# Kernel tuning notes

Hardware: AMD Instinct MI355X
Metric: run time of the kernel (lower is better)

Reference implementation:

```python
import jax, jax.numpy as jnp
import numpy as np

B, N = 16, 8192          # batch, number of points
IN_DIM, NDIM = 3, 2      # feature dim, spatial dim
K = 128                  # number of Fourier modes
C = 128                  # channel width (all layers equal)
L = 4                    # number of spectral layers
FC, OUT = 128, 1         # projection dims


def setup_inputs() -> dict:
    key = jax.random.key(0)
    ks = jax.random.split(key, 14)
    scale = 1.0 / (C * C)
    x = jax.random.uniform(ks[0], (B, N, IN_DIM + NDIM + 2), dtype=jnp.float32)
    modes = jax.random.normal(ks[1], (K, NDIM), dtype=jnp.float32) * (2.0 * jnp.pi)
    fc0_w = jax.random.normal(ks[2], (IN_DIM, C), dtype=jnp.float32) * 0.1
    fc0_b = jax.random.normal(ks[3], (C,), dtype=jnp.float32) * 0.1
    wc = scale * jax.random.uniform(ks[4], (L, C, C, K), dtype=jnp.float32)
    ws = scale * jax.random.uniform(ks[5], (L, C, C, K), dtype=jnp.float32)
    w0 = scale * jax.random.uniform(ks[6], (L, C, C, 1), dtype=jnp.float32)
    conv_w = jax.random.normal(ks[7], (L, C, C), dtype=jnp.float32) * 0.05  # Conv1d k=1 -> (out,in)
    conv_b = jax.random.normal(ks[8], (L, C), dtype=jnp.float32) * 0.05
    fc1_w = jax.random.normal(ks[9], (C, FC), dtype=jnp.float32) * 0.05
    fc1_b = jax.random.normal(ks[10], (FC,), dtype=jnp.float32) * 0.05
    fc2_w = jax.random.normal(ks[11], (FC, OUT), dtype=jnp.float32) * 0.05
    fc2_b = jax.random.normal(ks[12], (OUT,), dtype=jnp.float32) * 0.05
    return {"x": x, "modes": modes, "fc0_w": fc0_w, "fc0_b": fc0_b,
            "wc": wc, "ws": ws, "w0": w0, "conv_w": conv_w, "conv_b": conv_b,
            "fc1_w": fc1_w, "fc1_b": fc1_b, "fc2_w": fc2_w, "fc2_b": fc2_b}


def _gelu(v):
    return jax.nn.gelu(v, approximate=False)  # torch F.gelu default = exact erf


def reference(x, modes, fc0_w, fc0_b, wc, ws, w0, conv_w, conv_b, fc1_w, fc1_b, fc2_w, fc2_b):
    # aux channels: grid(ndim), weights(1), mask(1)
    aux = jnp.transpose(x[..., -(NDIM + 2):], (0, 2, 1))  # (b, ndim+2, N)
    grid = aux[:, :NDIM, :]
    weights = aux[:, NDIM:NDIM + 1, :]
    mask = aux[:, NDIM + 1:, :]
    size = grid.shape[-1]

    temp = jnp.einsum('bdx,kd->bkx', grid, modes)  # (b,k,N)
    bases_c = jnp.cos(temp) * mask
    bases_s = jnp.sin(temp) * mask
    bases_0 = mask                                  # (b,1,N)
    wsz = weights * size
    wbases_c, wbases_s, wbases_0 = bases_c * wsz, bases_s * wsz, bases_0 * wsz

    h = jnp.einsum('bxi,ic->bcx', x[..., :IN_DIM], fc0_w) + fc0_b[None, :, None]

    for l in range(L):
        # forward non-uniform transform
        x_c = jnp.einsum('bix,bkx->bik', h, wbases_c)
        x_s = -jnp.einsum('bix,bkx->bik', h, wbases_s)
        x_0 = jnp.einsum('bix,bkx->bik', h, wbases_0)
        Wc, Ws, W0 = wc[l] / size, ws[l] / size, w0[l] / size
        f_c = jnp.einsum('bik,iok->bok', x_c, Wc) - jnp.einsum('bik,iok->bok', x_s, Ws)
        f_s = jnp.einsum('bik,iok->bok', x_s, Wc) + jnp.einsum('bik,iok->bok', x_c, Ws)
        f_0 = jnp.einsum('bik,iok->bok', x_0, W0)
        # inverse transform
        x1 = (jnp.einsum('bok,bkx->box', f_0, bases_0)
              + 2.0 * jnp.einsum('bok,bkx->box', f_c, bases_c)
              - 2.0 * jnp.einsum('bok,bkx->box', f_s, bases_s))
        # pointwise 1x1 conv skip path
        x2 = jnp.einsum('oi,bix->box', conv_w[l], h) + conv_b[l][None, :, None]
        h = x1 + x2
        if l != L - 1:
            h = _gelu(h)

    y = jnp.transpose(h, (0, 2, 1))  # (b, N, C)
    y = _gelu(y @ fc1_w + fc1_b)
    y = y @ fc2_w + fc2_b
    return y
```

## Files before the change

kernel.cpp:

```cpp
#include <hip/hip_runtime.h>
#include <math.h>

#define BB 16
#define NN 8192
#define CC 128
#define KK 128
#define LL 4

#define APX 40
#define BPX 136

typedef short bf16x8 __attribute__((ext_vector_type(8)));
typedef float f32x4 __attribute__((ext_vector_type(4)));

typedef unsigned short u16;
typedef unsigned int u32;

__device__ __forceinline__ float gelu_f(float v){
  const float t = __builtin_amdgcn_exp2f(-2.45546696f * v);
  return v * __builtin_amdgcn_rcpf(1.0f + t);
}

__device__ __forceinline__ u16 f2bf(float f){
  u32 u = __float_as_uint(f);
  return (u16)((u + 0x7FFFu + ((u >> 16) & 1u)) >> 16);
}
__device__ __forceinline__ float bf2f(u16 u){ return __uint_as_float(((u32)u) << 16); }
__device__ __forceinline__ u32 pk2(float a, float b){
  return (u32)f2bf(a) | ((u32)f2bf(b) << 16);
}

__device__ __forceinline__ void gll16(const u16* g, u16* l){
  __builtin_amdgcn_global_load_lds(
      (const __attribute__((address_space(1))) void*)g,
      (__attribute__((address_space(3))) void*)l, 16, 0, 0);
}

__global__ __launch_bounds__(256) void bases_kernel(
    const float* __restrict__ X, const float* __restrict__ modes,
    u16* __restrict__ bcs, u16* __restrict__ bss,
    u16* __restrict__ bcT, u16* __restrict__ bsT,
    float* __restrict__ mA, float* __restrict__ sm2)
{
  __shared__ float smodes[2*KK];
  __shared__ u16 shc[64*BPX];
  __shared__ u16 shs[64*BPX];
  __shared__ float ssv[64];
  const int b = blockIdx.x;
  const int x0 = blockIdx.y*64;
  const int t = threadIdx.x;
  smodes[t] = modes[t];
  const int xl = t & 63;
  const int kq = t >> 6;
  const int x = x0 + xl;
  const float* xp = X + ((size_t)b*NN + x)*7;
  const float g0 = xp[3], g1 = xp[4], wv = xp[5], mv = xp[6];
  const float sv = wv * (float)NN;
  if (kq == 0){
    mA[b*NN + x] = mv;
    sm2[b*NN + x] = mv * sv;
    ssv[xl] = sv;
  }
  __syncthreads();
  #pragma unroll 4
  for (int kk = 0; kk < 32; ++kk){
    const int k = kq*32 + kk;
    const float tt = g0*smodes[2*k] + g1*smodes[2*k+1];
    float sn, cs;
    __sincosf(tt, &sn, &cs);
    shc[xl*BPX + k] = f2bf(cs*mv);
    shs[xl*BPX + k] = f2bf(sn*mv);
  }
  __syncthreads();
  for (int idx = t; idx < 64*16; idx += 256){
    const int row = idx >> 4, c16 = (idx & 15)*8;
    const size_t dst = ((size_t)b*NN + x0 + row)*KK + c16;
    *(uint4*)&bcT[dst] = *(const uint4*)&shc[row*BPX + c16];
    *(uint4*)&bsT[dst] = *(const uint4*)&shs[row*BPX + c16];
  }
  for (int idx = t; idx < 128*8; idx += 256){
    const int k = idx >> 3, x8 = (idx & 7)*8;
    uint4 vc, vs;
    u32* pc = (u32*)&vc;
    u32* ps = (u32*)&vs;
    #pragma unroll
    for (int e = 0; e < 4; ++e){
      const int xa = x8 + 2*e, xb2 = x8 + 2*e + 1;
      const float sa = ssv[xa], sb = ssv[xb2];
      pc[e] = pk2(bf2f(shc[xa*BPX+k])*sa, bf2f(shc[xb2*BPX+k])*sb);
      ps[e] = pk2(bf2f(shs[xa*BPX+k])*sa, bf2f(shs[xb2*BPX+k])*sb);
    }
    const size_t dst = ((size_t)b*KK + k)*NN + x0 + x8;
    *(uint4*)&bcs[dst] = vc;
    *(uint4*)&bss[dst] = vs;
  }
}

__global__ __launch_bounds__(256) void cvt_kernel(
    const float* __restrict__ convw, const float* __restrict__ fc1w,
    u16* __restrict__ cwb, u16* __restrict__ w1T)
{
  const int blk = blockIdx.x;
  const int t = threadIdx.x;
  if (blk < 64){
    const int base = blk*1024 + t*4;
    const float4 v = *(const float4*)&convw[base];
    ushort4 o;
    o.x = f2bf(v.x); o.y = f2bf(v.y); o.z = f2bf(v.z); o.w = f2bf(v.w);
    *(ushort4*)&cwb[base] = o;
  } else {
    const int i = (blk - 64)*1024 + t*4;
    const int f = i >> 7, c = i & 127;
    ushort4 o;
    o.x = f2bf(fc1w[(size_t)(c+0)*CC + f]);
    o.y = f2bf(fc1w[(size_t)(c+1)*CC + f]);
    o.z = f2bf(fc1w[(size_t)(c+2)*CC + f]);
    o.w = f2bf(fc1w[(size_t)(c+3)*CC + f]);
    *(ushort4*)&w1T[i] = o;
  }
}

__global__ __launch_bounds__(256) void fc0_kernel(
    const float* __restrict__ X, const float* __restrict__ w, const float* __restrict__ bias,
    const float* __restrict__ sm2,
    u16* __restrict__ hT, u16* __restrict__ hI, float* __restrict__ x0out)
{
  __shared__ float sxin[3*128];
  __shared__ float sw[3*128];
  __shared__ float sb[128];
  __shared__ float ssm2[128];
  __shared__ u16 sht[128*BPX];
  const int b = blockIdx.x;
  const int x0 = blockIdx.y*128;
  const int t = threadIdx.x;
  if (t < 128){
    sb[t] = bias[t];
    ssm2[t] = sm2[(size_t)b*NN + x0 + t];
    #pragma unroll
    for (int j = 0; j < 3; ++j){
      sw[j*128 + t] = w[j*128 + t];
      sxin[j*128 + t] = X[((size_t)b*NN + x0 + t)*7 + j];
    }
  }
  __syncthreads();
  const int o = t >> 1;
  const int xh = (t & 1)*64;
  const float w0v = sw[o], w1v = sw[128+o], w2v = sw[256+o], bv = sb[o];
  float xacc = 0.f;
  for (int x = xh; x < xh + 64; ++x){
    const float v = bv + sxin[x]*w0v + sxin[128+x]*w1v + sxin[256+x]*w2v;
    sht[o*BPX + x] = f2bf(v);
    xacc += v * ssm2[x];
  }
  xacc += __shfl_xor(xacc, 1);
  if ((t & 1) == 0) atomicAdd(&x0out[b*CC + o], xacc);
  __syncthreads();
  for (int idx = t; idx < 128*16; idx += 256){
    const int o2 = idx >> 4, x8 = (idx & 15)*8;
    *(uint4*)&hI[((size_t)b*CC + o2)*NN + x0 + x8] = *(const uint4*)&sht[o2*BPX + x8];
  }
  {
    const int x = t >> 1, oh = (t & 1)*64;
    #pragma unroll 2
    for (int j = 0; j < 8; ++j){
      const int ob = oh + j*8;
      uint4 qv;
      qv.x = (u32)sht[(ob+0)*BPX + x] | ((u32)sht[(ob+1)*BPX + x] << 16);
      qv.y = (u32)sht[(ob+2)*BPX + x] | ((u32)sht[(ob+3)*BPX + x] << 16);
      qv.z = (u32)sht[(ob+4)*BPX + x] | ((u32)sht[(ob+5)*BPX + x] << 16);
      qv.w = (u32)sht[(ob+6)*BPX + x] | ((u32)sht[(ob+7)*BPX + x] << 16);
      *(uint4*)&hT[((size_t)b*NN + x0 + x)*CC + ob] = qv;
    }
  }
}

template<int STORE>
__global__ __launch_bounds__(256) void proj_kernel(
    const u16* __restrict__ hI, const u16* __restrict__ bcs, const u16* __restrict__ bss,
    float* __restrict__ xc, float* __restrict__ xs)
{
  __shared__ u16 sa [2][128*32];
  __shared__ u16 sbc[2][128*32];
  __shared__ u16 sbs[2][128*32];
  const int b = blockIdx.x;
  const int z = blockIdx.y;
  const int t = threadIdx.x;
  const int w = t >> 6, l = t & 63, lm = l & 15, q = l >> 4;
  const int rr = l >> 2, c8 = (l & 3)*8;
  const u16* Asrc = hI + (size_t)b*CC*NN + z*512;
  const u16* Bc   = bcs + (size_t)b*KK*NN + z*512;
  const u16* Bs   = bss + (size_t)b*KK*NN + z*512;
  const f32x4 z4 = {0.f,0.f,0.f,0.f};
  f32x4 accC[2][8], accS[2][8];
  #pragma unroll
  for (int mt = 0; mt < 2; ++mt)
    #pragma unroll
    for (int nt = 0; nt < 8; ++nt){ accC[mt][nt] = z4; accS[mt][nt] = z4; }

  #pragma unroll
  for (int j = 0; j < 2; ++j){
    const int r = w*32 + j*16 + rr;
    gll16(Asrc + (size_t)r*NN + c8, sa [0] + (w*32 + j*16)*32);
    gll16(Bc   + (size_t)r*NN + c8, sbc[0] + (w*32 + j*16)*32);
    gll16(Bs   + (size_t)r*NN + c8, sbs[0] + (w*32 + j*16)*32);
  }
  for (int cs = 0; cs < 16; ++cs){
    __syncthreads();
    const int cur = cs & 1;
    if (cs < 15){
      const int nb = cur ^ 1;
      const int c2 = (cs + 1)*32;
      #pragma unroll
      for (int j = 0; j < 2; ++j){
        const int r = w*32 + j*16 + rr;
        gll16(Asrc + (size_t)r*NN + c2 + c8, sa [nb] + (w*32 + j*16)*32);
        gll16(Bc   + (size_t)r*NN + c2 + c8, sbc[nb] + (w*32 + j*16)*32);
        gll16(Bs   + (size_t)r*NN + c2 + c8, sbs[nb] + (w*32 + j*16)*32);
      }
    }
    const bf16x8 af0 = *(const bf16x8*)&sa[cur][(w*32      + lm)*32 + q*8];
    const bf16x8 af1 = *(const bf16x8*)&sa[cur][(w*32 + 16 + lm)*32 + q*8];
    #pragma unroll
    for (int nt = 0; nt < 8; ++nt){
      const bf16x8 bfc = *(const bf16x8*)&sbc[cur][(nt*16 + lm)*32 + q*8];
      const bf16x8 bfs = *(const bf16x8*)&sbs[cur][(nt*16 + lm)*32 + q*8];
      accC[0][nt] = __builtin_amdgcn_mfma_f32_16x16x32_bf16(af0, bfc, accC[0][nt], 0, 0, 0);
      accC[1][nt] = __builtin_amdgcn_mfma_f32_16x16x32_bf16(af1, bfc, accC[1][nt], 0, 0, 0);
      accS[0][nt] = __builtin_amdgcn_mfma_f32_16x16x32_bf16(af0, bfs, accS[0][nt], 0, 0, 0);
      accS[1][nt] = __builtin_amdgcn_mfma_f32_16x16x32_bf16(af1, bfs, accS[1][nt], 0, 0, 0);
    }
  }
  if (STORE){
    const size_t pbase = ((size_t)z*BB + b)*CC*KK;
    #pragma unroll
    for (int mt = 0; mt < 2; ++mt){
      #pragma unroll
      for (int nt = 0; nt < 8; ++nt){
        const int k = nt*16 + lm;
        #pragma unroll
        for (int r = 0; r < 4; ++r){
          const int i = w*32 + mt*16 + q*4 + r;
          xc[pbase + (size_t)i*KK + k] = accC[mt][nt][r];
          xs[pbase + (size_t)i*KK + k] = accS[mt][nt][r];
        }
      }
    }
  } else {
    #pragma unroll
    for (int mt = 0; mt < 2; ++mt){
      #pragma unroll
      for (int nt = 0; nt < 8; ++nt){
        const int k = nt*16 + lm;
        #pragma unroll
        for (int r = 0; r < 4; ++r){
          const int i = w*32 + mt*16 + q*4 + r;
          atomicAdd(&xc[((size_t)b*CC + i)*KK + k],  accC[mt][nt][r]);
          atomicAdd(&xs[((size_t)b*CC + i)*KK + k], -accS[mt][nt][r]);
        }
      }
    }
  }
}

__global__ __launch_bounds__(128) void reduce_f0_kernel(
    const float* __restrict__ xcP, const float* __restrict__ xsP,
    float* __restrict__ xc, float* __restrict__ xs,
    const float* __restrict__ x0a, const float* __restrict__ w0l,
    float* __restrict__ f0b)
{
  const int blk = blockIdx.x;
  if (blk < 2048){
    const int k = threadIdx.x;
    const size_t off = (size_t)blk*KK + k;
    const size_t zstr = (size_t)BB*CC*KK;
    float sc_ = 0.f, ss_ = 0.f;
    #pragma unroll
    for (int z = 0; z < 16; ++z){
      sc_ += xcP[(size_t)z*zstr + off];
      ss_ += xsP[(size_t)z*zstr + off];
    }
    xc[off] = sc_;
    xs[off] = -ss_;
  } else {
    const int b = blk - 2048, o = threadIdx.x;
    float acc = 0.f;
    for (int i = 0; i < CC; ++i) acc += x0a[b*CC+i] * w0l[(size_t)i*CC + o];
    f0b[b*CC+o] = acc * (1.0f/(float)NN);
  }
}

__global__ __launch_bounds__(128) void f0_kernel(
    const float* __restrict__ x0a, const float* __restrict__ w0l, float* __restrict__ f0b)
{
  const int b = blockIdx.x, o = threadIdx.x;
  float acc = 0.f;
  for (int i = 0; i < CC; ++i) acc += x0a[b*CC+i] * w0l[(size_t)i*CC + o];
  f0b[b*CC+o] = acc * (1.0f/(float)NN);
}

__global__ __launch_bounds__(256) void mix_kernel(
    const float* __restrict__ xc, const float* __restrict__ xs,
    const float* __restrict__ wcl, const float* __restrict__ wsl,
    u16* __restrict__ fcb, u16* __restrict__ fsb)
{
  const int o  = blockIdx.x;
  const int kh = blockIdx.y;
  const int t = threadIdx.x;
  const int k = kh*64 + (t & 63);
  const int bq = t >> 6;
  float aC[4] = {0.f,0.f,0.f,0.f}, aS[4] = {0.f,0.f,0.f,0.f};
  const float* wcp = wcl + (size_t)o*KK + k;
  const float* wsp = wsl + (size_t)o*KK + k;
  const float* xcp = xc + ((size_t)(bq*4)*CC)*KK + k;
  const float* xsp = xs + ((size_t)(bq*4)*CC)*KK + k;
  #pragma unroll 2
  for (int i = 0; i < CC; ++i){
    const float wcv = wcp[(size_t)i*CC*KK];
    const float wsv = wsp[(size_t)i*CC*KK];
    #pragma unroll
    for (int jb = 0; jb < 4; ++jb){
      const float xcv = xcp[((size_t)jb*CC + i)*KK];
      const float xsv = xsp[((size_t)jb*CC + i)*KK];
      aC[jb] += xcv*wcv - xsv*wsv;
      aS[jb] += xsv*wcv + xcv*wsv;
    }
  }
  const float sc = 2.0f/(float)NN;
  #pragma unroll
  for (int jb = 0; jb < 4; ++jb){
    const int b = bq*4 + jb;
    fcb[((size_t)b*CC + o)*KK + k] = f2bf( aC[jb]*sc);
    fsb[((size_t)b*CC + o)*KK + k] = f2bf(-aS[jb]*sc);
  }
}

__global__ __launch_bounds__(512) void fused_kernel(
    const u16* __restrict__ bcT, const u16* __restrict__ bsT, u16* __restrict__ hT,
    const u16* __restrict__ fcb, const u16* __restrict__ fsb,
    const u16* __restrict__ cwb, const float* __restrict__ cb,
    const float* __restrict__ f0b, const float* __restrict__ mA, const float* __restrict__ sm2,
    u16* __restrict__ hI, float* __restrict__ x0next, const int act)
{
  __shared__ u16 smem[24576];
  __shared__ float sm[256], ssm2[256], sf0[128], scb[128];
  const int b  = blockIdx.x;
  const int x0 = blockIdx.y*256;
  const int t = threadIdx.x;
  const int w = t >> 6, l = t & 63, lm = l & 15, q = l >> 4;
  const int lr = l >> 2, lc8 = (l & 3)*8;
  if (t < 256){
    sm[t]   = mA[(size_t)b*NN + x0 + t];
    ssm2[t] = sm2[(size_t)b*NN + x0 + t];
  }
  if (t < 128){
    sf0[t]  = f0b[b*CC + t];
    scb[t]  = cb[t];
  }
  const u16* Asrc0 = bcT + ((size_t)b*NN + x0)*KK;
  const u16* Asrc1 = bsT + ((size_t)b*NN + x0)*KK;
  const u16* Asrc2 = hT  + ((size_t)b*NN + x0)*CC;
  const u16* Bsrc0 = fcb + (size_t)b*CC*KK;
  const u16* Bsrc1 = fsb + (size_t)b*CC*KK;
  const f32x4 z4 = {0.f,0.f,0.f,0.f};
  f32x4 acc[2][8];
  #pragma unroll
  for (int mt = 0; mt < 2; ++mt)
    #pragma unroll
    for (int nt = 0; nt < 8; ++nt) acc[mt][nt] = z4;

  {
    const int ar = w*16 + lr;
    gll16(Asrc0 + (size_t)ar*128 + lc8,         smem + w*512);
    gll16(Asrc0 + (size_t)(ar+128)*128 + lc8,   smem + 4096 + w*512);
    gll16(Bsrc0 + (size_t)ar*128 + lc8,         smem + 16384 + w*512);
  }
  for (int s = 0; s < 12; ++s){
    __syncthreads();
    const int curA = (s & 1)*8192;
    const int curB = 16384 + (s & 1)*4096;
    if (s < 11){
      const int s1 = s + 1;
      const int g = s1 >> 2, kk = (s1 & 3)*32;
      const u16* Ap = (g == 0) ? Asrc0 : (g == 1) ? Asrc1 : Asrc2;
      const u16* Bp = (g == 0) ? Bsrc0 : (g == 1) ? Bsrc1 : cwb;
      const int nbA = (s1 & 1)*8192;
      const int nbB = 16384 + (s1 & 1)*4096;
      const int ar = w*16 + lr;
      gll16(Ap + (size_t)ar*128 + kk + lc8,       smem + nbA + w*512);
      gll16(Ap + (size_t)(ar+128)*128 + kk + lc8, smem + nbA + 4096 + w*512);
      gll16(Bp + (size_t)ar*128 + kk + lc8,       smem + nbB + w*512);
    }
    const bf16x8 af0 = *(const bf16x8*)&smem[curA + (w*32      + lm)*32 + q*8];
    const bf16x8 af1 = *(const bf16x8*)&smem[curA + (w*32 + 16 + lm)*32 + q*8];
    #pragma unroll
    for (int nt = 0; nt < 8; ++nt){
      const bf16x8 bf = *(const bf16x8*)&smem[curB + (nt*16 + lm)*32 + q*8];
      acc[0][nt] = __builtin_amdgcn_mfma_f32_16x16x32_bf16(af0, bf, acc[0][nt], 0, 0, 0);
      acc[1][nt] = __builtin_amdgcn_mfma_f32_16x16x32_bf16(af1, bf, acc[1][nt], 0, 0, 0);
    }
  }
  #pragma unroll
  for (int pass = 0; pass < 2; ++pass){
    __syncthreads();
    if ((w >> 2) == pass){
      float xpart[8];
      #pragma unroll
      for (int nt = 0; nt < 8; ++nt) xpart[nt] = 0.f;
      const int wl = w & 3;
      #pragma unroll
      for (int mt = 0; mt < 2; ++mt){
        const int xg = w*32 + mt*16 + q*4;
        const int xl = wl*32 + mt*16 + q*4;
        #pragma unroll
        for (int nt = 0; nt < 8; ++nt){
          const int o = nt*16 + lm;
          const float f0v = sf0[o], cbv = scb[o];
          float v0 = acc[mt][nt][0] + f0v*sm[xg+0] + cbv;
          float v1 = acc[mt][nt][1] + f0v*sm[xg+1] + cbv;
          float v2 = acc[mt][nt][2] + f0v*sm[xg+2] + cbv;
          float v3 = acc[mt][nt][3] + f0v*sm[xg+3] + cbv;
          if (act){ v0 = gelu_f(v0); v1 = gelu_f(v1); v2 = gelu_f(v2); v3 = gelu_f(v3); }
          smem[(xl+0)*BPX + o] = f2bf(v0);
          smem[(xl+1)*BPX + o] = f2bf(v1);
          smem[(xl+2)*BPX + o] = f2bf(v2);
          smem[(xl+3)*BPX + o] = f2bf(v3);
          if (act){
            uint2 st;
            st.x = pk2(v0, v1);
            st.y = pk2(v2, v3);
            *(uint2*)&hI[((size_t)b*CC + o)*NN + x0 + xg] = st;
            xpart[nt] += v0*ssm2[xg+0] + v1*ssm2[xg+1] + v2*ssm2[xg+2] + v3*ssm2[xg+3];
          }
        }
      }
      if (act){
        #pragma unroll
        for (int nt = 0; nt < 8; ++nt){
          float v = xpart[nt];
          v += __shfl_xor(v, 16);
          v += __shfl_xor(v, 32);
          if (q == 0) atomicAdd(&x0next[b*CC + nt*16 + lm], v);
        }
      }
    }
    __syncthreads();
    {
      const int xr = t >> 2;
      const int oq = (t & 3)*32;
      const size_t dst = ((size_t)b*NN + x0 + pass*128 + xr)*CC + oq;
      #pragma unroll
      for (int j = 0; j < 4; ++j){
        const uint4 v = *(const uint4*)&smem[xr*BPX + oq + j*8];
        *(uint4*)&hT[dst + j*8] = v;
      }
    }
  }
}

__global__ __launch_bounds__(256) void final_kernel(
    const u16* __restrict__ hT, const u16* __restrict__ w1T,
    const float* __restrict__ b1, const float* __restrict__ w2, const float* __restrict__ b2,
    float* __restrict__ out)
{
  __shared__ u16 sa[128*APX];
  __shared__ u16 sbt[128*APX];
  __shared__ float sb1[128], sw2[128];
  const int b  = blockIdx.x;
  const int x0 = blockIdx.y*128;
  const int t = threadIdx.x;
  const int w = t >> 6, l = t & 63, lm = l & 15, q = l >> 4;
  if (t < 128){ sb1[t] = b1[t]; sw2[t] = w2[t]; }
  const float b2v = b2[0];
  const f32x4 z4 = {0.f,0.f,0.f,0.f};
  f32x4 acc[2][8];
  #pragma unroll
  for (int mt = 0; mt < 2; ++mt)
    #pragma unroll
    for (int nt = 0; nt < 8; ++nt) acc[mt][nt] = z4;
  const u16* Ap = hT + ((size_t)b*NN + x0)*CC;
  const int row = t >> 2, ch = (t & 3)*8;
  for (int s = 0; s < 4; ++s){
    const int kk = s*32;
    __syncthreads();
    #pragma unroll
    for (int h = 0; h < 2; ++h){
      const int r = row + h*64;
      *(uint4*)&sa [r*APX + ch] = *(const uint4*)&Ap [(size_t)r*CC + kk + ch];
      *(uint4*)&sbt[r*APX + ch] = *(const uint4*)&w1T[(size_t)r*CC + kk + ch];
    }
    __syncthreads();
    bf16x8 af[2];
    af[0] = *(const bf16x8*)&sa[(w*32      + lm)*APX + q*8];
    af[1] = *(const bf16x8*)&sa[(w*32 + 16 + lm)*APX + q*8];
    #pragma unroll
    for (int nt = 0; nt < 8; ++nt){
      const bf16x8 bf = *(const bf16x8*)&sbt[(nt*16 + lm)*APX + q*8];
      acc[0][nt] = __builtin_amdgcn_mfma_f32_16x16x32_bf16(af[0], bf, acc[0][nt], 0, 0, 0);
      acc[1][nt] = __builtin_amdgcn_mfma_f32_16x16x32_bf16(af[1], bf, acc[1][nt], 0, 0, 0);
    }
  }
  #pragma unroll
  for (int mt = 0; mt < 2; ++mt){
    #pragma unroll
    for (int r = 0; r < 4; ++r){
      float s = 0.f;
      #pragma unroll
      for (int nt = 0; nt < 8; ++nt){
        const int f = nt*16 + lm;
        s += gelu_f(acc[mt][nt][r] + sb1[f]) * sw2[f];
      }
      s += __shfl_xor(s, 1);
      s += __shfl_xor(s, 2);
      s += __shfl_xor(s, 4);
      s += __shfl_xor(s, 8);
      if (lm == 0){
        const int x = x0 + w*32 + mt*16 + q*4 + r;
        out[(size_t)b*NN + x] = s + b2v;
      }
    }
  }
}

extern "C" void kernel_launch(void* const* d_in, const int* in_sizes, int n_in,
                              void* d_out, int out_size, void* d_ws, size_t ws_size,
                              hipStream_t stream)
{
  const float* X     = (const float*)d_in[0];
  const float* modes = (const float*)d_in[1];
  const float* fc0w  = (const float*)d_in[2];
  const float* fc0b  = (const float*)d_in[3];
  const float* wc    = (const float*)d_in[4];
  const float* wsm   = (const float*)d_in[5];
  const float* w0    = (const float*)d_in[6];
  const float* convw = (const float*)d_in[7];
  const float* convb = (const float*)d_in[8];
  const float* fc1w  = (const float*)d_in[9];
  const float* fc1b  = (const float*)d_in[10];
  const float* fc2w  = (const float*)d_in[11];
  const float* fc2b  = (const float*)d_in[12];
  float* out = (float*)d_out;

  const size_t nBKN = (size_t)BB*KK*NN;
  const size_t nBCK = (size_t)BB*CC*KK;
  const size_t nBC  = (size_t)BB*CC;
  const size_t nBN  = (size_t)BB*NN;

  const size_t need_A = 6*nBKN*2 + 2*(size_t)16*nBCK*4 + 2*nBCK*4 + 4*nBC*4
                      + 2*nBCK*2 + nBC*4 + 2*nBN*4 + (size_t)LL*CC*CC*2 + (size_t)CC*CC*2;
  const bool pathA = (ws_size >= need_A);

  char* p = (char*)d_ws;
  u16* bcs = (u16*)p; p += nBKN*2;
  u16* bss = (u16*)p; p += nBKN*2;
  u16* bcT = (u16*)p; p += nBKN*2;
  u16* bsT = (u16*)p; p += nBKN*2;
  u16* hI  = (u16*)p; p += nBKN*2;
  u16* hT  = (u16*)p; p += nBKN*2;
  float* xcP = nullptr; float* xsP = nullptr;
  if (pathA){
    xcP = (float*)p; p += (size_t)16*nBCK*4;
    xsP = (float*)p; p += (size_t)16*nBCK*4;
  }
  float* xcA = (float*)p; p += nBCK*4;
  float* xsA = (float*)p; p += nBCK*4;
  float* x0A = (float*)p; p += 4*nBC*4;
  u16* fcb = (u16*)p; p += nBCK*2;
  u16* fsb = (u16*)p; p += nBCK*2;
  float* f0b = (float*)p; p += nBC*4;
  float* mA  = (float*)p; p += nBN*4;
  float* sm2 = (float*)p; p += nBN*4;
  u16* cwb = (u16*)p; p += (size_t)LL*CC*CC*2;
  u16* w1T = (u16*)p; p += (size_t)CC*CC*2;

  hipMemsetAsync(x0A, 0, 4*nBC*sizeof(float), stream);
  cvt_kernel<<<dim3(80), 256, 0, stream>>>(convw, fc1w, cwb, w1T);
  bases_kernel<<<dim3(BB, NN/64), 256, 0, stream>>>(X, modes, bcs, bss, bcT, bsT, mA, sm2);
  fc0_kernel<<<dim3(BB, NN/128), 256, 0, stream>>>(X, fc0w, fc0b, sm2, hT, hI, x0A);

  for (int l = 0; l < LL; ++l){
    if (pathA){
      proj_kernel<1><<<dim3(BB, 16), 256, 0, stream>>>(hI, bcs, bss, xcP, xsP);
      reduce_f0_kernel<<<dim3(2048 + BB), 128, 0, stream>>>(xcP, xsP, xcA, xsA,
          x0A + (size_t)l*nBC, w0 + (size_t)l*CC*CC, f0b);
    } else {
      hipMemsetAsync(xcA, 0, 2*nBCK*sizeof(float), stream);
      proj_kernel<0><<<dim3(BB, 16), 256, 0, stream>>>(hI, bcs, bss, xcA, xsA);
      f0_kernel<<<dim3(BB), 128, 0, stream>>>(x0A + (size_t)l*nBC, w0 + (size_t)l*CC*CC, f0b);
    }
    mix_kernel<<<dim3(128, 2), 256, 0, stream>>>(xcA, xsA,
        wc + (size_t)l*CC*CC*KK, wsm + (size_t)l*CC*CC*KK, fcb, fsb);
    fused_kernel<<<dim3(BB, NN/256), 512, 0, stream>>>(
        bcT, bsT, hT, fcb, fsb,
        cwb + (size_t)l*CC*CC, convb + (size_t)l*CC,
        f0b, mA, sm2, hI,
        x0A + (size_t)(l+1 < LL ? l+1 : 0)*nBC,
        (l < LL-1) ? 1 : 0);
  }
  final_kernel<<<dim3(BB, NN/128), 256, 0, stream>>>(hT, w1T, fc1b, fc2w, fc2b, out);
}
```

Before: 711.7 us.

## Split projection kernel into cos/sin blocks with 512 threads each

The partial-sum projection path now launches a 512-thread kernel over a third grid dimension that selects the cosine or sine basis. Each block loads only the h tile and one basis tile and computes a single accumulator set per wave. This doubles the block count and cuts registers per thread, which should raise occupancy and parallelism. The cost is that the h tile is loaded twice, once per kind, which adds global traffic. The atomic path keeps the old kernel under a new name.

```diff
diff --git a/kernel.cpp b/kernel.cpp
--- a/kernel.cpp
+++ b/kernel.cpp
@@ -174,8 +174,57 @@
   }
 }
 
-template<int STORE>
-__global__ __launch_bounds__(256) void proj_kernel(
+__global__ __launch_bounds__(512) void proj512_kernel(
+    const u16* __restrict__ hI, const u16* __restrict__ bcs, const u16* __restrict__ bss,
+    float* __restrict__ xcP, float* __restrict__ xsP)
+{
+  __shared__ u16 sa[2][128*32];
+  __shared__ u16 sb[2][128*32];
+  const int b = blockIdx.x;
+  const int z = blockIdx.y;
+  const int kind = blockIdx.z;
+  const int t = threadIdx.x;
+  const int w = t >> 6, l = t & 63, lm = l & 15, q = l >> 4;
+  const int ar = t >> 2, ac8 = (t & 3)*8;
+  const u16* Asrc = hI + (size_t)b*CC*NN + z*512;
+  const u16* Bsrc = (kind ? bss : bcs) + (size_t)b*KK*NN + z*512;
+  const f32x4 z4 = {0.f,0.f,0.f,0.f};
+  f32x4 acc[8];
+  #pragma unroll
+  for (int nt = 0; nt < 8; ++nt) acc[nt] = z4;
+
+  gll16(Asrc + (size_t)ar*NN + ac8, sa[0] + w*512);
+  gll16(Bsrc + (size_t)ar*NN + ac8, sb[0] + w*512);
+  for (int cs = 0; cs < 16; ++cs){
+    __syncthreads();
+    const int cur = cs & 1;
+    if (cs < 15){
+      const int nb = cur ^ 1;
+      const int c2 = (cs + 1)*32;
+      gll16(Asrc + (size_t)ar*NN + c2 + ac8, sa[nb] + w*512);
+      gll16(Bsrc + (size_t)ar*NN + c2 + ac8, sb[nb] + w*512);
+    }
+    const bf16x8 af = *(const bf16x8*)&sa[cur][(w*16 + lm)*32 + q*8];
+    #pragma unroll
+    for (int nt = 0; nt < 8; ++nt){
+      const bf16x8 bf = *(const bf16x8*)&sb[cur][(nt*16 + lm)*32 + q*8];
+      acc[nt] = __builtin_amdgcn_mfma_f32_16x16x32_bf16(af, bf, acc[nt], 0, 0, 0);
+    }
+  }
+  float* outp = kind ? xsP : xcP;
+  const size_t pbase = ((size_t)z*BB + b)*CC*KK;
+  #pragma unroll
+  for (int nt = 0; nt < 8; ++nt){
+    const int k = nt*16 + lm;
+    #pragma unroll
+    for (int r = 0; r < 4; ++r){
+      const int i = w*16 + q*4 + r;
+      outp[pbase + (size_t)i*KK + k] = acc[nt][r];
+    }
+  }
+}
+
+__global__ __launch_bounds__(256) void proj_atomic_kernel(
     const u16* __restrict__ hI, const u16* __restrict__ bcs, const u16* __restrict__ bss,
     float* __restrict__ xc, float* __restrict__ xs)
 {
@@ -196,7 +245,6 @@
   for (int mt = 0; mt < 2; ++mt)
     #pragma unroll
     for (int nt = 0; nt < 8; ++nt){ accC[mt][nt] = z4; accS[mt][nt] = z4; }
-
   #pragma unroll
   for (int j = 0; j < 2; ++j){
     const int r = w*32 + j*16 + rr;
@@ -230,33 +278,16 @@
       accS[1][nt] = __builtin_amdgcn_mfma_f32_16x16x32_bf16(af1, bfs, accS[1][nt], 0, 0, 0);
     }
   }
-  if (STORE){
-    const size_t pbase = ((size_t)z*BB + b)*CC*KK;
-    #pragma unroll
-    for (int mt = 0; mt < 2; ++mt){
+  #pragma unroll
+  for (int mt = 0; mt < 2; ++mt){
+    #pragma unroll
+    for (int nt = 0; nt < 8; ++nt){
+      const int k = nt*16 + lm;
       #pragma unroll
-      for (int nt = 0; nt < 8; ++nt){
-        const int k = nt*16 + lm;
-        #pragma unroll
-        for (int r = 0; r < 4; ++r){
-          const int i = w*32 + mt*16 + q*4 + r;
-          xc[pbase + (size_t)i*KK + k] = accC[mt][nt][r];
-          xs[pbase + (size_t)i*KK + k] = accS[mt][nt][r];
-        }
-      }
-    }
-  } else {
-    #pragma unroll
-    for (int mt = 0; mt < 2; ++mt){
-      #pragma unroll
-      for (int nt = 0; nt < 8; ++nt){
-        const int k = nt*16 + lm;
-        #pragma unroll
-        for (int r = 0; r < 4; ++r){
-          const int i = w*32 + mt*16 + q*4 + r;
-          atomicAdd(&xc[((size_t)b*CC + i)*KK + k],  accC[mt][nt][r]);
-          atomicAdd(&xs[((size_t)b*CC + i)*KK + k], -accS[mt][nt][r]);
-        }
+      for (int r = 0; r < 4; ++r){
+        const int i = w*32 + mt*16 + q*4 + r;
+        atomicAdd(&xc[((size_t)b*CC + i)*KK + k],  accC[mt][nt][r]);
+        atomicAdd(&xs[((size_t)b*CC + i)*KK + k], -accS[mt][nt][r]);
       }
     }
   }
@@ -579,12 +610,12 @@
 
   for (int l = 0; l < LL; ++l){
     if (pathA){
-      proj_kernel<1><<<dim3(BB, 16), 256, 0, stream>>>(hI, bcs, bss, xcP, xsP);
+      proj512_kernel<<<dim3(BB, 16, 2), 512, 0, stream>>>(hI, bcs, bss, xcP, xsP);
       reduce_f0_kernel<<<dim3(2048 + BB), 128, 0, stream>>>(xcP, xsP, xcA, xsA,
           x0A + (size_t)l*nBC, w0 + (size_t)l*CC*CC, f0b);
     } else {
       hipMemsetAsync(xcA, 0, 2*nBCK*sizeof(float), stream);
-      proj_kernel<0><<<dim3(BB, 16), 256, 0, stream>>>(hI, bcs, bss, xcA, xsA);
+      proj_atomic_kernel<<<dim3(BB, 16), 256, 0, stream>>>(hI, bcs, bss, xcA, xsA);
       f0_kernel<<<dim3(BB), 128, 0, stream>>>(x0A + (size_t)l*nBC, w0 + (size_t)l*CC*CC, f0b);
     }
     mix_kernel<<<dim3(128, 2), 256, 0, stream>>>(xcA, xsA,
```

After: 679.4 us. 1.05x faster.
